# Kernel optimization log

Hardware: AMD Instinct MI355X
Metric: run time of the kernel (lower is better)

Reference implementation:

```python
import jax, jax.numpy as jnp
import numpy as np

B1, B2, CHUNK, HID, T = 64, 16, 128, 64, 131072
N_CHUNKS = 128


def setup_inputs() -> dict:
    key = jax.random.key(0)
    ks = jax.random.split(key, 12)
    # positive prices so log(p) is finite
    p = jax.random.uniform(ks[0], (T, 2), jnp.float32) * 2.0 + 0.5
    inds = jax.random.randint(ks[1], (B1,), 0, 100000, dtype=jnp.int32)
    open_slices = jax.random.randint(ks[2], (B1, B2, 1), 0, T, dtype=jnp.int32)
    ls_probs = jax.random.uniform(ks[3], (B1, B2, 1, 1), jnp.float32)
    open_probs = jax.random.uniform(ks[4], (B1, B2, 1, 1), jnp.float32)
    open_hx = jax.random.normal(ks[5], (B1, B2, 2, HID), jnp.float32) * 0.1
    s = 1.0 / np.sqrt(HID)
    # torch nn.LSTM params: gate order i,f,g,o
    W_ih = jax.random.uniform(ks[6], (4 * HID, 2), jnp.float32, -s, s)
    W_hh = jax.random.uniform(ks[7], (4 * HID, HID), jnp.float32, -s, s)
    b_ih = jax.random.uniform(ks[8], (4 * HID,), jnp.float32, -s, s)
    b_hh = jax.random.uniform(ks[9], (4 * HID,), jnp.float32, -s, s)
    W_out = jax.random.uniform(ks[10], (1, HID), jnp.float32, -s, s)
    b_out = jax.random.uniform(ks[11], (1,), jnp.float32, -s, s)
    return {"inds": inds, "p": p, "ls_probs": ls_probs, "open_probs": open_probs,
            "open_slices": open_slices, "open_hx": open_hx,
            "W_ih": W_ih, "W_hh": W_hh, "b_ih": b_ih, "b_hh": b_hh,
            "W_out": W_out, "b_out": b_out, "n_chunks": N_CHUNKS}


def reference(inds, p, ls_probs, open_probs, open_slices, open_hx,
              W_ih, W_hh, b_ih, b_hh, W_out, b_out, n_chunks):
    b1, b2 = open_hx.shape[:2]
    hid = open_hx.shape[-1]
    C = CHUNK
    h0 = open_hx[:, :, 0, :].reshape(b1 * b2, hid)
    c0 = open_hx[:, :, 1, :].reshape(b1 * b2, hid)
    open_logp = jnp.log(p[open_slices])  # (b1, b2, 1, 2)
    # sliding-window gather base: idx[i,j,t] = inds[i] + j + t (per-chunk offset added in scan)
    base = (inds[:, None, None]
            + jnp.arange(b2, dtype=inds.dtype)[None, :, None]
            + jnp.arange(C, dtype=inds.dtype)[None, None, :])  # (b1, b2, C)
    bias = b_ih + b_hh

    def lstm_chunk(x, h, c):  # x: (N, C, 2)
        xg = x @ W_ih.T + bias  # precompute input projection: (N, C, 4H)
        def step(carry, xg_t):
            h, c = carry
            g = xg_t + h @ W_hh.T
            i, f, gg, o = jnp.split(g, 4, axis=-1)
            c = jax.nn.sigmoid(f) * c + jax.nn.sigmoid(i) * jnp.tanh(gg)
            h = jax.nn.sigmoid(o) * jnp.tanh(c)
            return (h, c), h
        (h, c), hs = jax.lax.scan(step, (h, c), xg.swapaxes(0, 1))
        return hs.swapaxes(0, 1), h, c  # (N, C, H)

    def chunk_step(carry, offset):
        h, c, last_nd, loss = carry
        idx = base + offset * C                      # (b1, b2, C)
        p_chunk = p[idx]                             # (b1, b2, C, 2)
        x = p_chunk - p_chunk[:, :, :1, :]           # re-center on first step of chunk
        out, h, c = lstm_chunk(x.reshape(b1 * b2, C, 2), h, c)
        probs = jax.nn.sigmoid(out.reshape(b1, b2, C, hid) @ W_out.T + b_out)  # (b1,b2,C,1)
        not_done = last_nd * jnp.cumprod(1.0 - probs[:, :, :-1], axis=2)       # (b1,b2,C-1,1)
        probs = jnp.concatenate([probs[:, :, :1], probs[:, :, 1:] * not_done], axis=2)
        last_nd = not_done[:, :, -1:, :]
        logp = jnp.log(p_chunk)
        payoff = ls_probs * (logp - open_logp) + (1.0 - ls_probs) * (open_logp - logp)
        loss = loss + jnp.sum(open_probs * probs * payoff)
        return (h, c, last_nd, loss), None

    init = (h0, c0, jnp.ones((b1, b2, 1, 1), p.dtype), jnp.zeros((), p.dtype))
    (_, _, _, loss), _ = jax.lax.scan(chunk_step, init, jnp.arange(n_chunks))
    return loss
```

## Files before the change

### kernel.cpp

```cpp
#include <hip/hip_runtime.h>


#define CH   128
#define HID  64
#define HSTR 72

typedef __fp16 f16x8 __attribute__((ext_vector_type(8)));
typedef float  f32x4 __attribute__((ext_vector_type(4)));

#define MFMA16(a, b, c) __builtin_amdgcn_mfma_f32_16x16x32_f16((a), (b), (c), 0, 0, 0)

#define DPP_ADD(v, C) ((v) + __builtin_bit_cast(float, \
    __builtin_amdgcn_update_dpp(0, __builtin_bit_cast(int, (v)), (C), 0xF, 0xF, true)))

__device__ __forceinline__ float frcp(float x) { return __builtin_amdgcn_rcpf(x); }
__device__ __forceinline__ float sigm(float x) { return frcp(1.0f + __expf(-x)); }
__device__ __forceinline__ float tanh_(float x) {
  float e = __expf(2.0f * x);
  return 1.0f - 2.0f * frcp(e + 1.0f);
}

__global__ __launch_bounds__(256, 1)
void pc_lstm_kernel(const int* __restrict__ inds,
                    const float* __restrict__ p,
                    const float* __restrict__ ls_probs,
                    const float* __restrict__ open_probs,
                    const int* __restrict__ open_slices,
                    const float* __restrict__ open_hx,
                    const float* __restrict__ W_ih,
                    const float* __restrict__ W_hh,
                    const float* __restrict__ b_ih,
                    const float* __restrict__ b_hh,
                    const float* __restrict__ W_out,
                    const float* __restrict__ b_out,
                    const int* __restrict__ n_chunks_p,
                    float* __restrict__ out)
{
  __shared__ __align__(16) __fp16 hbuf[2][16 * HSTR];
  __shared__ __align__(16) float2 xbuf[2][4][CH];
  __shared__ __align__(16) float  ltbuf[2][4][CH];
  __shared__ __align__(16) float  zbuf[2][4][4];
  __shared__ __align__(16) float  scat[4][4][16][4];

  const int tid  = threadIdx.x;
  const int w    = tid >> 6;
  const int lane = tid & 63;
  const int q    = lane >> 4;
  const int lm   = lane & 15;
  const int wg   = blockIdx.x;
  const int n_chunks = n_chunks_p[0];
  const int total = n_chunks * CH;

  const int hid_own = 16 * w + lm;
  const int sg_own  = wg * 4 + q;

  f16x8 Bf[4][2];
#pragma unroll
  for (int g = 0; g < 4; ++g)
#pragma unroll
    for (int kh = 0; kh < 2; ++kh) {
      const float* src = W_hh + (g * HID + hid_own) * HID + kh * 32 + q * 8;
      f16x8 b;
#pragma unroll
      for (int j = 0; j < 8; ++j) b[j] = (__fp16)src[j];
      Bf[g][kh] = b;
    }

  float wxa[4], wxb[4], bb[4];
#pragma unroll
  for (int g = 0; g < 4; ++g) {
    const int row = g * HID + hid_own;
    wxa[g] = W_ih[2 * row];
    wxb[g] = W_ih[2 * row + 1];
    bb[g]  = b_ih[row] + b_hh[row];
  }
  const float wo   = W_out[hid_own];
  const float bout = b_out[0];

  float cst = open_hx[(sg_own * 2 + 1) * HID + hid_own];
  const float h0 = open_hx[(sg_own * 2 + 0) * HID + hid_own];

  {
    __fp16* hb = &hbuf[0][0];
    for (int i = tid; i < 2 * 16 * HSTR; i += 256) hb[i] = (__fp16)0.0f;
  }
  __syncthreads();
  hbuf[0][q * HSTR + hid_own] = (__fp16)h0;

  const int sg_q = wg * 4 + q;
  const int tb_q = inds[sg_q >> 4] + (sg_q & 15);

  const int   sg_w  = wg * 4 + w;
  const int   osw   = open_slices[sg_w];
  const float OLw   = __logf(p[2 * osw]) + __logf(p[2 * osw + 1]);
  const float coefw = open_probs[sg_w] * (2.0f * ls_probs[sg_w] - 1.0f);

  float Sd = 1.0f, Qd = 1.0f, lsum = 0.0f, psum = 0.0f;
  const float2* p2 = (const float2*)p;

  auto lagged_loss = [&](int lgt) {
    const int ltt = lgt & (CH - 1);
    const int lcb = (lgt >> 7) & 1;
    const float4 zz = *(const float4*)&zbuf[lgt & 1][w][0];
    const float pr = sigm(zz.x + zz.y + zz.z + zz.w + bout);
    const float Lt = ltbuf[lcb][w][ltt];
    if (ltt == 0) Qd = 1.0f;
    const float T  = (ltt == 0) ? 1.0f : Sd * Qd;
    const float pn = pr * T;
    lsum = fmaf(pn, Lt, lsum);
    psum += pn;
    if (ltt == CH - 1) Sd *= Qd;
    Qd *= (1.0f - pr);
  };

  for (int gt = 0; gt < total; ++gt) {
    const int tt = gt & (CH - 1);
    const int cb = (gt >> 7) & 1;

    if (tt == 0) {
      const int tb2 = tb_q + (gt >> 7) * CH;
      const float2 pb = p2[tb2];
#pragma unroll
      for (int r = 0; r < 2; ++r) {
        const int t = 32 * w + 16 * r + lm;
        const float2 pt = p2[tb2 + t];
        float2 xv; xv.x = pt.x - pb.x; xv.y = pt.y - pb.y;
        xbuf[cb][q][t]  = xv;
        ltbuf[cb][q][t] = __logf(pt.x) + __logf(pt.y);
      }
      __syncthreads();
    }

    const __fp16* hrow = &hbuf[gt & 1][lm * HSTR];
    const f16x8 a0 = *(const f16x8*)(hrow + q * 8);
    const f16x8 a1 = *(const f16x8*)(hrow + 32 + q * 8);

    f32x4 zero4 = {0.0f, 0.0f, 0.0f, 0.0f};
    f32x4 C0 = MFMA16(a0, Bf[0][0], zero4); C0 = MFMA16(a1, Bf[0][1], C0);
    f32x4 C1 = MFMA16(a0, Bf[1][0], zero4); C1 = MFMA16(a1, Bf[1][1], C1);
    f32x4 C2 = MFMA16(a0, Bf[2][0], zero4); C2 = MFMA16(a1, Bf[2][1], C2);
    f32x4 C3 = MFMA16(a0, Bf[3][0], zero4); C3 = MFMA16(a1, Bf[3][1], C3);

    if (gt > 0) lagged_loss(gt - 1);

    if (lane < 16) {
      *(f32x4*)&scat[w][0][lane][0] = C0;
      *(f32x4*)&scat[w][1][lane][0] = C1;
      *(f32x4*)&scat[w][2][lane][0] = C2;
      *(f32x4*)&scat[w][3][lane][0] = C3;
    }
    const float2 xv = xbuf[cb][q][tt];
    float pa[4];
#pragma unroll
    for (int g = 0; g < 4; ++g) {
      const float cg = scat[w][g][lm][q];
      pa[g] = fmaf(xv.y, wxb[g], fmaf(xv.x, wxa[g], cg + bb[g]));
    }

    const float ig = sigm(pa[0]);
    const float fg = sigm(pa[1]);
    const float gg = tanh_(pa[2]);
    const float og = sigm(pa[3]);
    cst = fmaf(fg, cst, ig * gg);
    const float h = og * tanh_(cst);

    hbuf[(gt + 1) & 1][q * HSTR + hid_own] = (__fp16)h;

    float zp = h * wo;
    zp = DPP_ADD(zp, 0x111);
    zp = DPP_ADD(zp, 0x112);
    zp = DPP_ADD(zp, 0x114);
    zp = DPP_ADD(zp, 0x118);
    if (lm == 15) zbuf[gt & 1][q][w] = zp;

    __syncthreads();
  }

  lagged_loss(total - 1);

  if (lane == 0) atomicAdd(out, coefw * (lsum - OLw * psum));
}

extern "C" void kernel_launch(void* const* d_in, const int* in_sizes, int n_in,
                              void* d_out, int out_size, void* d_ws, size_t ws_size,
                              hipStream_t stream) {
  (void)hipMemsetAsync(d_out, 0, sizeof(float), stream);

  pc_lstm_kernel<<<dim3(256), dim3(256), 0, stream>>>(
      (const int*)d_in[0],
      (const float*)d_in[1],
      (const float*)d_in[2],
      (const float*)d_in[3],
      (const int*)d_in[4],
      (const float*)d_in[5],
      (const float*)d_in[6],
      (const float*)d_in[7],
      (const float*)d_in[8],
      (const float*)d_in[9],
      (const float*)d_in[10],
      (const float*)d_in[11],
      (const int*)d_in[12],
      (float*)d_out);
}
```

Measured before the change: 8.166 ms.

## Run one LSTM sequence per wavefront with register-only h exchange

Each wavefront now owns a whole sequence and computes all 256 gate columns itself with 32 MFMAs per step. The hidden state is broadcast through ds_bpermute and readlane instead of LDS buffers and block-wide barriers. The output projection is folded into an extra MFMA, and prices are prefetched one chunk ahead into registers. The aim is to remove the per-step __syncthreads and LDS round trips from the serial recurrence. In exchange each wave issues four times more MFMAs, most of whose rows are redundant, and does more cross-lane permutes per step.

```diff
diff --git a/kernel.cpp b/kernel.cpp
--- a/kernel.cpp
+++ b/kernel.cpp
@@ -1,18 +1,30 @@
 #include <hip/hip_runtime.h>
 
 
-#define CH   128
-#define HID  64
-#define HSTR 72
+#define CH  128
+#define HID 64
 
 typedef __fp16 f16x8 __attribute__((ext_vector_type(8)));
+typedef __fp16 f16x2 __attribute__((ext_vector_type(2)));
 typedef float  f32x4 __attribute__((ext_vector_type(4)));
+typedef int    i32x4 __attribute__((ext_vector_type(4)));
 
 #define MFMA16(a, b, c) __builtin_amdgcn_mfma_f32_16x16x32_f16((a), (b), (c), 0, 0, 0)
 
-#define DPP_ADD(v, C) ((v) + __builtin_bit_cast(float, \
-    __builtin_amdgcn_update_dpp(0, __builtin_bit_cast(int, (v)), (C), 0xF, 0xF, true)))
-
+__device__ __forceinline__ float rlf(float v, int l) {
+  return __builtin_bit_cast(float, __builtin_amdgcn_readlane(__builtin_bit_cast(int, v), l));
+}
+__device__ __forceinline__ int packh(float a, float b) {
+  f16x2 v = __builtin_amdgcn_cvt_pkrtz(a, b);
+  return __builtin_bit_cast(int, v);
+}
+__device__ __forceinline__ int bperm(int byteaddr, int src) {
+  return __builtin_amdgcn_ds_bpermute(byteaddr, src);
+}
+__device__ __forceinline__ float bpermf(int byteaddr, float src) {
+  return __builtin_bit_cast(float,
+      __builtin_amdgcn_ds_bpermute(byteaddr, __builtin_bit_cast(int, src)));
+}
 __device__ __forceinline__ float frcp(float x) { return __builtin_amdgcn_rcpf(x); }
 __device__ __forceinline__ float sigm(float x) { return frcp(1.0f + __expf(-x)); }
 __device__ __forceinline__ float tanh_(float x) {
@@ -36,149 +48,157 @@
                     const int* __restrict__ n_chunks_p,
                     float* __restrict__ out)
 {
-  __shared__ __align__(16) __fp16 hbuf[2][16 * HSTR];
-  __shared__ __align__(16) float2 xbuf[2][4][CH];
-  __shared__ __align__(16) float  ltbuf[2][4][CH];
-  __shared__ __align__(16) float  zbuf[2][4][4];
-  __shared__ __align__(16) float  scat[4][4][16][4];
-
-  const int tid  = threadIdx.x;
-  const int w    = tid >> 6;
-  const int lane = tid & 63;
+  const int lane = threadIdx.x & 63;
+  const int w    = threadIdx.x >> 6;
+  const int s    = blockIdx.x * 4 + w;
   const int q    = lane >> 4;
   const int lm   = lane & 15;
-  const int wg   = blockIdx.x;
   const int n_chunks = n_chunks_p[0];
-  const int total = n_chunks * CH;
-
-  const int hid_own = 16 * w + lm;
-  const int sg_own  = wg * 4 + q;
-
-  f16x8 Bf[4][2];
+
+  f16x8 Bf[4][4][2];
 #pragma unroll
   for (int g = 0; g < 4; ++g)
 #pragma unroll
-    for (int kh = 0; kh < 2; ++kh) {
-      const float* src = W_hh + (g * HID + hid_own) * HID + kh * 32 + q * 8;
-      f16x8 b;
-#pragma unroll
-      for (int j = 0; j < 8; ++j) b[j] = (__fp16)src[j];
-      Bf[g][kh] = b;
-    }
+    for (int cb = 0; cb < 4; ++cb)
+#pragma unroll
+      for (int kh = 0; kh < 2; ++kh) {
+        const float* src = W_hh + (g * HID + 16 * cb + lm) * HID + 32 * kh + 8 * q;
+        f16x8 b;
+#pragma unroll
+        for (int j = 0; j < 8; ++j) b[j] = (__fp16)src[j];
+        Bf[g][cb][kh] = b;
+      }
+  f16x8 Bz[2];
+#pragma unroll
+  for (int kh = 0; kh < 2; ++kh) {
+    f16x8 b;
+#pragma unroll
+    for (int j = 0; j < 8; ++j)
+      b[j] = (lm == 0) ? (__fp16)W_out[32 * kh + 8 * q + j] : (__fp16)0.0f;
+    Bz[kh] = b;
+  }
 
   float wxa[4], wxb[4], bb[4];
 #pragma unroll
   for (int g = 0; g < 4; ++g) {
-    const int row = g * HID + hid_own;
+    const int row = g * HID + lane;
     wxa[g] = W_ih[2 * row];
     wxb[g] = W_ih[2 * row + 1];
     bb[g]  = b_ih[row] + b_hh[row];
   }
-  const float wo   = W_out[hid_own];
+  const float wo   = W_out[lane];
   const float bout = b_out[0];
 
-  float cst = open_hx[(sg_own * 2 + 1) * HID + hid_own];
-  const float h0 = open_hx[(sg_own * 2 + 0) * HID + hid_own];
+  float h = open_hx[(s * 2 + 0) * HID + lane];
+  float c = open_hx[(s * 2 + 1) * HID + lane];
+  const int   os   = open_slices[s];
+  const float OL   = __logf(p[2 * os]) + __logf(p[2 * os + 1]);
+  const float coef = open_probs[s] * (2.0f * ls_probs[s] - 1.0f);
+  const int   tbase = inds[s >> 4] + (s & 15);
+
+  int aadr0[4], aadr1[4];
+#pragma unroll
+  for (int m = 0; m < 4; ++m) {
+    aadr0[m] = 8 * (4 * q + m);
+    aadr1[m] = 8 * (16 + 4 * q + m);
+  }
+  const int dadr = 4 * lm;
+
+  float Sd = 1.0f, Qd = 1.0f, lsum = 0.0f, psum = 0.0f;
+  float Lcarry = 0.0f;
+  float LBprev = 0.0f;
+
+  const float2* p2 = (const float2*)p;
+  float2 curA = p2[tbase + lane];
+  float2 curB = p2[tbase + HID + lane];
+  float2 nxtA = curA, nxtB = curB;
+
+  for (int off = 0; off < n_chunks; ++off) {
+    if (off) { Lcarry = rlf(LBprev, 63); curA = nxtA; curB = nxtB; }
+    const float LA = __logf(curA.x) + __logf(curA.y);
+    const float LB = __logf(curB.x) + __logf(curB.y);
+    const float px0 = rlf(curA.x, 0);
+    const float px1 = rlf(curA.y, 0);
+    if (off + 1 < n_chunks) {
+      const int nb = tbase + (off + 1) * CH;
+      nxtA = p2[nb + lane];
+      nxtB = p2[nb + HID + lane];
+    }
+
+#pragma unroll 1
+    for (int tt = 0; tt < CH; ++tt) {
+      const int hp = packh(h, __shfl_xor(h, 1, 64));
+      i32x4 t0, t1;
+#pragma unroll
+      for (int m = 0; m < 4; ++m) {
+        t0[m] = bperm(aadr0[m], hp);
+        t1[m] = bperm(aadr1[m], hp);
+      }
+      const f16x8 a0 = __builtin_bit_cast(f16x8, t0);
+      const f16x8 a1 = __builtin_bit_cast(f16x8, t1);
+
+      const f32x4 zero4 = {0.0f, 0.0f, 0.0f, 0.0f};
+      f32x4 Cz = MFMA16(a0, Bz[0], zero4);
+      Cz = MFMA16(a1, Bz[1], Cz);
+
+      float pre[4];
+#pragma unroll
+      for (int g = 0; g < 4; ++g) {
+        f32x4 C0 = MFMA16(a0, Bf[g][0][0], zero4); C0 = MFMA16(a1, Bf[g][0][1], C0);
+        f32x4 C1 = MFMA16(a0, Bf[g][1][0], zero4); C1 = MFMA16(a1, Bf[g][1][1], C1);
+        f32x4 C2 = MFMA16(a0, Bf[g][2][0], zero4); C2 = MFMA16(a1, Bf[g][2][1], C2);
+        f32x4 C3 = MFMA16(a0, Bf[g][3][0], zero4); C3 = MFMA16(a1, Bf[g][3][1], C3);
+        const float r0 = bpermf(dadr, C0[0]);
+        const float r1 = bpermf(dadr, C1[0]);
+        const float r2 = bpermf(dadr, C2[0]);
+        const float r3 = bpermf(dadr, C3[0]);
+        pre[g] = (q == 0) ? r0 : (q == 1) ? r1 : (q == 2) ? r2 : r3;
+      }
+
+      const float zprev = rlf(Cz[0], 0);
+      if (off | tt) {
+        const int ltt = (tt == 0) ? (CH - 1) : (tt - 1);
+        const float Lt = (tt == 0) ? Lcarry
+                       : (ltt < 64) ? rlf(LA, ltt) : rlf(LB, ltt - 64);
+        const float pr = sigm(zprev + bout);
+        if (ltt == 0) Qd = 1.0f;
+        const float T  = (ltt == 0) ? 1.0f : Sd * Qd;
+        const float pn = pr * T;
+        lsum = fmaf(pn, Lt, lsum);
+        psum += pn;
+        if (ltt == CH - 1) Sd *= Qd;
+        Qd *= (1.0f - pr);
+      }
+
+      const float sp0 = (tt < 64) ? rlf(curA.x, tt) : rlf(curB.x, tt & 63);
+      const float sp1 = (tt < 64) ? rlf(curA.y, tt) : rlf(curB.y, tt & 63);
+      const float x0 = sp0 - px0;
+      const float x1 = sp1 - px1;
+#pragma unroll
+      for (int g = 0; g < 4; ++g)
+        pre[g] = fmaf(x1, wxb[g], fmaf(x0, wxa[g], pre[g] + bb[g]));
+
+      const float ig = sigm(pre[0]);
+      const float fg = sigm(pre[1]);
+      const float gg = tanh_(pre[2]);
+      const float og = sigm(pre[3]);
+      c = fmaf(fg, c, ig * gg);
+      h = og * tanh_(c);
+    }
+    LBprev = LB;
+  }
 
   {
-    __fp16* hb = &hbuf[0][0];
-    for (int i = tid; i < 2 * 16 * HSTR; i += 256) hb[i] = (__fp16)0.0f;
-  }
-  __syncthreads();
-  hbuf[0][q * HSTR + hid_own] = (__fp16)h0;
-
-  const int sg_q = wg * 4 + q;
-  const int tb_q = inds[sg_q >> 4] + (sg_q & 15);
-
-  const int   sg_w  = wg * 4 + w;
-  const int   osw   = open_slices[sg_w];
-  const float OLw   = __logf(p[2 * osw]) + __logf(p[2 * osw + 1]);
-  const float coefw = open_probs[sg_w] * (2.0f * ls_probs[sg_w] - 1.0f);
-
-  float Sd = 1.0f, Qd = 1.0f, lsum = 0.0f, psum = 0.0f;
-  const float2* p2 = (const float2*)p;
-
-  auto lagged_loss = [&](int lgt) {
-    const int ltt = lgt & (CH - 1);
-    const int lcb = (lgt >> 7) & 1;
-    const float4 zz = *(const float4*)&zbuf[lgt & 1][w][0];
-    const float pr = sigm(zz.x + zz.y + zz.z + zz.w + bout);
-    const float Lt = ltbuf[lcb][w][ltt];
-    if (ltt == 0) Qd = 1.0f;
-    const float T  = (ltt == 0) ? 1.0f : Sd * Qd;
-    const float pn = pr * T;
-    lsum = fmaf(pn, Lt, lsum);
+    float zp = h * wo;
+#pragma unroll
+    for (int m = 32; m > 0; m >>= 1) zp += __shfl_xor(zp, m, 64);
+    const float pr = sigm(zp + bout);
+    const float pn = pr * Sd * Qd;
+    lsum = fmaf(pn, rlf(LBprev, 63), lsum);
     psum += pn;
-    if (ltt == CH - 1) Sd *= Qd;
-    Qd *= (1.0f - pr);
-  };
-
-  for (int gt = 0; gt < total; ++gt) {
-    const int tt = gt & (CH - 1);
-    const int cb = (gt >> 7) & 1;
-
-    if (tt == 0) {
-      const int tb2 = tb_q + (gt >> 7) * CH;
-      const float2 pb = p2[tb2];
-#pragma unroll
-      for (int r = 0; r < 2; ++r) {
-        const int t = 32 * w + 16 * r + lm;
-        const float2 pt = p2[tb2 + t];
-        float2 xv; xv.x = pt.x - pb.x; xv.y = pt.y - pb.y;
-        xbuf[cb][q][t]  = xv;
-        ltbuf[cb][q][t] = __logf(pt.x) + __logf(pt.y);
-      }
-      __syncthreads();
-    }
-
-    const __fp16* hrow = &hbuf[gt & 1][lm * HSTR];
-    const f16x8 a0 = *(const f16x8*)(hrow + q * 8);
-    const f16x8 a1 = *(const f16x8*)(hrow + 32 + q * 8);
-
-    f32x4 zero4 = {0.0f, 0.0f, 0.0f, 0.0f};
-    f32x4 C0 = MFMA16(a0, Bf[0][0], zero4); C0 = MFMA16(a1, Bf[0][1], C0);
-    f32x4 C1 = MFMA16(a0, Bf[1][0], zero4); C1 = MFMA16(a1, Bf[1][1], C1);
-    f32x4 C2 = MFMA16(a0, Bf[2][0], zero4); C2 = MFMA16(a1, Bf[2][1], C2);
-    f32x4 C3 = MFMA16(a0, Bf[3][0], zero4); C3 = MFMA16(a1, Bf[3][1], C3);
-
-    if (gt > 0) lagged_loss(gt - 1);
-
-    if (lane < 16) {
-      *(f32x4*)&scat[w][0][lane][0] = C0;
-      *(f32x4*)&scat[w][1][lane][0] = C1;
-      *(f32x4*)&scat[w][2][lane][0] = C2;
-      *(f32x4*)&scat[w][3][lane][0] = C3;
-    }
-    const float2 xv = xbuf[cb][q][tt];
-    float pa[4];
-#pragma unroll
-    for (int g = 0; g < 4; ++g) {
-      const float cg = scat[w][g][lm][q];
-      pa[g] = fmaf(xv.y, wxb[g], fmaf(xv.x, wxa[g], cg + bb[g]));
-    }
-
-    const float ig = sigm(pa[0]);
-    const float fg = sigm(pa[1]);
-    const float gg = tanh_(pa[2]);
-    const float og = sigm(pa[3]);
-    cst = fmaf(fg, cst, ig * gg);
-    const float h = og * tanh_(cst);
-
-    hbuf[(gt + 1) & 1][q * HSTR + hid_own] = (__fp16)h;
-
-    float zp = h * wo;
-    zp = DPP_ADD(zp, 0x111);
-    zp = DPP_ADD(zp, 0x112);
-    zp = DPP_ADD(zp, 0x114);
-    zp = DPP_ADD(zp, 0x118);
-    if (lm == 15) zbuf[gt & 1][q][w] = zp;
-
-    __syncthreads();
-  }
-
-  lagged_loss(total - 1);
-
-  if (lane == 0) atomicAdd(out, coefw * (lsum - OLw * psum));
+  }
+
+  if (lane == 0) atomicAdd(out, coef * (lsum - OL * psum));
 }
 
 extern "C" void kernel_launch(void* const* d_in, const int* in_sizes, int n_in,
```

Result: slower. 12.21 ms (+49.5%).
